# Kernel optimization log

Hardware: AMD Instinct MI355X
Metric: run time of the kernel (lower is better)

The kernel has to match this reference:

```python
import jax, jax.numpy as jnp
import numpy as np

INF, OUTF, BIT, GROUPSIZE = 4096, 11008, 4, 128
GROUPS = INF // GROUPSIZE  # 32
PACK = 32 // BIT           # 8 values per int32


def setup_inputs() -> dict:
    key = jax.random.key(0)
    k1, k2, k3, k4, k5 = jax.random.split(key, 5)
    x = jax.random.normal(k1, (2, 2048, INF), dtype=jnp.float32)
    # packed 4-bit weights: (INF*BIT/32, OUTF) int32
    qweight = jax.random.randint(k2, (INF * BIT // 32, OUTF), 0, 2147483647, dtype=jnp.int32)
    scales = jax.random.uniform(k3, (OUTF, GROUPS, 1), dtype=jnp.float32) * 0.01 + 0.001
    zeros = jax.random.uniform(k4, (OUTF, GROUPS, 1), dtype=jnp.float32) * 0.1
    bias = jax.random.normal(k5, (OUTF,), dtype=jnp.float32)
    return {"x": x, "qweight": qweight, "scales": scales, "zeros": zeros, "bias": bias}


def _dequant(qweight, scales, zeros):
    # unpack 8 nibbles per int32 row -> intweight (INF, OUTF)
    shifts = (BIT * jnp.arange(PACK, dtype=jnp.int32))[None, :, None]  # (1,8,1)
    nibbles = (qweight[:, None, :] >> shifts) & 0xF                    # (INF/8, 8, OUTF)
    wq = nibbles.reshape(INF, OUTF).astype(jnp.float32)
    # per-group dequant: W[k,n] = q*scale[n, k//gs] - zero[n, k//gs]
    s = scales[:, :, 0].T[:, None, :]  # (GROUPS, 1, OUTF)
    z = zeros[:, :, 0].T[:, None, :]
    w = wq.reshape(GROUPS, GROUPSIZE, OUTF) * s - z
    return w.reshape(INF, OUTF)


def reference(x, qweight, scales, zeros, bias):
    w = _dequant(qweight, scales, zeros)  # (INF, OUTF)
    # y = x @ W + bias  (matches y init to bias then vecquant4matmul accumulate)
    return jnp.einsum('bsk,kn->bsn', x, w) + bias
```

## Files before the change

### kernel.cpp

```cpp
#include <hip/hip_runtime.h>
#include <hip/hip_bf16.h>
#include <cstdint>
#include <cstddef>

#define K_DIM   4096
#define N_DIM   11008
#define M_DIM   4096
#define GROUPS  32
#define QROWS   512

typedef __bf16 bf16x8 __attribute__((ext_vector_type(8)));
typedef float  f32x4  __attribute__((ext_vector_type(4)));

__device__ __forceinline__ void async16(const void* g, void* lds) {
    __builtin_amdgcn_global_load_lds(
        (const __attribute__((address_space(1))) uint32_t*)g,
        (__attribute__((address_space(3))) uint32_t*)lds,
        16, 0, 0);
}

#define DQ_NN   64
#define DQ_KK   32
#define DQ_ROW  264
__global__ __launch_bounds__(256) void dequant_kernel(
        const uint32_t* __restrict__ qw,
        const float* __restrict__ scales,
        const float* __restrict__ zeros,
        __bf16* __restrict__ Wt) {
    __shared__ __align__(16) __bf16 T[DQ_NN * DQ_ROW];

    const int n0  = blockIdx.x * DQ_NN;
    const int kk0 = blockIdx.y * DQ_KK;
    const int tid = threadIdx.x;

#pragma unroll
    for (int it = 0; it < 8; ++it) {
        const int flat = it * 256 + tid;
        const int kk_l = flat >> 6;
        const int n_l  = flat & 63;
        const int kk   = kk0 + kk_l;
        const int n    = n0 + n_l;
        const uint32_t q = qw[(size_t)kk * N_DIM + n];
        const int g = kk >> 4;
        const float s = scales[(size_t)n * GROUPS + g];
        const float z = zeros[(size_t)n * GROUPS + g];
        bf16x8 w;
#pragma unroll
        for (int j = 0; j < 8; ++j) {
            float v = (float)((q >> (4 * j)) & 0xF) * s - z;
            w[j] = (__bf16)v;
        }
        *(bf16x8*)(&T[n_l * DQ_ROW + kk_l * 8]) = w;
    }
    __syncthreads();

#pragma unroll
    for (int it = 0; it < 8; ++it) {
        const int flat = it * 256 + tid;
        const int n_l    = flat >> 5;
        const int kchunk = flat & 31;
        bf16x8 v = *(const bf16x8*)(&T[n_l * DQ_ROW + kchunk * 8]);
        *(bf16x8*)(Wt + (size_t)(n0 + n_l) * K_DIM + (size_t)kk0 * 8 + kchunk * 8) = v;
    }
}

__global__ __launch_bounds__(256) void xconv_kernel(
        const float* __restrict__ x, __bf16* __restrict__ xb) {
    const size_t i = ((size_t)blockIdx.x * 256 + threadIdx.x) * 8;
    const float4* p = (const float4*)(x + i);
    float4 a = p[0];
    float4 b = p[1];
    bf16x8 o;
    o[0] = (__bf16)a.x; o[1] = (__bf16)a.y; o[2] = (__bf16)a.z; o[3] = (__bf16)a.w;
    o[4] = (__bf16)b.x; o[5] = (__bf16)b.y; o[6] = (__bf16)b.z; o[7] = (__bf16)b.w;
    *(bf16x8*)(xb + i) = o;
}

#define GN 86
#define GM 32
#define SN 16
__global__ __launch_bounds__(256, 4) void gemm_kernel(
        const __bf16* __restrict__ A,
        const __bf16* __restrict__ Bt,
        const float* __restrict__ bias,
        float* __restrict__ C) {
    __shared__ __align__(16) __bf16 As[128 * 32];
    __shared__ __align__(16) __bf16 Bs[128 * 32];

    const int tid  = threadIdx.x;
    const int wave = tid >> 6;
    const int lane = tid & 63;
    const int wm   = wave >> 1;
    const int wn   = wave & 1;
    const int quad = lane >> 4;
    const int l16  = lane & 15;

    const int bid = blockIdx.x;
    const int g   = bid >> 9;
    const int rem = bid & 511;
    int n_t, m_t;
    const int snw = (GN - g * SN) < SN ? (GN - g * SN) : SN;
    if (snw == SN) { n_t = g * SN + (rem & (SN - 1)); m_t = rem >> 4; }
    else           { n_t = g * SN + rem % snw;        m_t = rem / snw; }

    const int m0 = m_t * 128;
    const int n0 = n_t * 128;

    f32x4 acc[4][4] = {};

    const int c0 = wave * 128 + lane;
    const int c1 = c0 + 64;
    const __bf16* gA0 = A  + (size_t)(m0 + (c0 >> 2)) * K_DIM + (c0 & 3) * 8;
    const __bf16* gA1 = A  + (size_t)(m0 + (c1 >> 2)) * K_DIM + (c1 & 3) * 8;
    const __bf16* gB0 = Bt + (size_t)(n0 + (c0 >> 2)) * K_DIM + (c0 & 3) * 8;
    const __bf16* gB1 = Bt + (size_t)(n0 + (c1 >> 2)) * K_DIM + (c1 & 3) * 8;
    char* ldsA0 = (char*)As + (wave * 2 + 0) * 1024;
    char* ldsA1 = (char*)As + (wave * 2 + 1) * 1024;
    char* ldsB0 = (char*)Bs + (wave * 2 + 0) * 1024;
    char* ldsB1 = (char*)Bs + (wave * 2 + 1) * 1024;

    const __bf16* la = As + ((size_t)(wm * 64 + l16)) * 32 + quad * 8;
    const __bf16* lb = Bs + ((size_t)(wn * 64 + l16)) * 32 + quad * 8;

    for (int kt = 0; kt < K_DIM / 32; ++kt) {
        async16(gA0, ldsA0);
        async16(gA1, ldsA1);
        async16(gB0, ldsB0);
        async16(gB1, ldsB1);
        gA0 += 32; gA1 += 32; gB0 += 32; gB1 += 32;
        __syncthreads();

        bf16x8 af[4], bf[4];
#pragma unroll
        for (int i = 0; i < 4; ++i) af[i] = *(const bf16x8*)(la + i * 16 * 32);
#pragma unroll
        for (int i = 0; i < 4; ++i) bf[i] = *(const bf16x8*)(lb + i * 16 * 32);

#pragma unroll
        for (int i = 0; i < 4; ++i)
#pragma unroll
            for (int j = 0; j < 4; ++j)
                acc[i][j] = __builtin_amdgcn_mfma_f32_16x16x32_bf16(
                    af[i], bf[j], acc[i][j], 0, 0, 0);

        __syncthreads();
    }

#pragma unroll
    for (int j = 0; j < 4; ++j) {
        const int n = n0 + wn * 64 + j * 16 + l16;
        const float bv = bias[n];
#pragma unroll
        for (int i = 0; i < 4; ++i) {
            const int mb = m0 + wm * 64 + i * 16 + quad * 4;
#pragma unroll
            for (int r = 0; r < 4; ++r) {
                C[(size_t)(mb + r) * N_DIM + n] = acc[i][j][r] + bv;
            }
        }
    }
}

extern "C" void kernel_launch(void* const* d_in, const int* in_sizes, int n_in,
                              void* d_out, int out_size, void* d_ws, size_t ws_size,
                              hipStream_t stream) {
    const float*    x      = (const float*)d_in[0];
    const uint32_t* qw     = (const uint32_t*)d_in[1];
    const float*    scales = (const float*)d_in[2];
    const float*    zeros  = (const float*)d_in[3];
    const float*    bias   = (const float*)d_in[4];
    float*          out    = (float*)d_out;

    __bf16* Wt = (__bf16*)d_ws;
    __bf16* xb = (__bf16*)((char*)d_ws + (size_t)N_DIM * K_DIM * sizeof(__bf16));

    dim3 dq_grid(N_DIM / DQ_NN, QROWS / DQ_KK);
    dequant_kernel<<<dq_grid, 256, 0, stream>>>(qw, scales, zeros, Wt);
    xconv_kernel<<<(M_DIM * K_DIM) / (256 * 8), 256, 0, stream>>>(x, xb);

    gemm_kernel<<<GN * GM, 256, 0, stream>>>(xb, Wt, bias, out);
}
```

Baseline: 703.0 us.

## Rewrite GEMM with 256x256 tiles, double-buffered swizzled LDS and interleaved async staging

Replaces the 128x128x32 single-buffered GEMM with a 256x256x64 tile kernel using 8 waves. Global-to-LDS async loads for the next K-tile are spread across the MFMA phases, with explicit vmcnt waits and raw barriers, so memory traffic overlaps compute. LDS columns are XOR-swizzled to avoid bank conflicts, blocks are remapped across XCDs, and setprio raises MFMA priority. The larger tiles raise arithmetic intensity but use 128KB of LDS and many accumulator registers, which limits occupancy to a few blocks per CU.

```diff
diff --git a/kernel.cpp b/kernel.cpp
--- a/kernel.cpp
+++ b/kernel.cpp
@@ -18,6 +18,9 @@
         (__attribute__((address_space(3))) uint32_t*)lds,
         16, 0, 0);
 }
+
+#define FENCE() asm volatile("" ::: "memory")
+#define BAR()   do { FENCE(); __builtin_amdgcn_s_barrier(); FENCE(); } while (0)
 
 #define DQ_NN   64
 #define DQ_KK   32
@@ -76,87 +79,160 @@
     *(bf16x8*)(xb + i) = o;
 }
 
-#define GN 86
-#define GM 32
-#define SN 16
-__global__ __launch_bounds__(256, 4) void gemm_kernel(
+#define BM 256
+#define BN 256
+#define BK 64
+#define NT 43
+#define MT 16
+#define NWG (NT*MT)
+
+#define PH_BODY(MF, J0, J1)                                                   \
+    do {                                                                      \
+        bf16x8 aLk0 = *(const bf16x8*)(ar0 + (MF)*1024);                      \
+        bf16x8 aLk1 = *(const bf16x8*)(ar1 + (MF)*1024);                      \
+        bf16x8 aHk0 = *(const bf16x8*)(ar0 + ((MF)+1)*1024);                  \
+        bf16x8 aHk1 = *(const bf16x8*)(ar1 + ((MF)+1)*1024);                  \
+        if constexpr (DO_STAGE) {                                             \
+            async16(gsrc[(J0)], lds + ldst[(J0)] + soff);                     \
+            async16(gsrc[(J1)], lds + ldst[(J1)] + soff);                     \
+        }                                                                     \
+        BAR();                                                                \
+        __builtin_amdgcn_s_setprio(1);                                        \
+        acc[(MF)  ][0] = __builtin_amdgcn_mfma_f32_16x16x32_bf16(aLk0, b0k0, acc[(MF)  ][0], 0,0,0); \
+        acc[(MF)  ][1] = __builtin_amdgcn_mfma_f32_16x16x32_bf16(aLk0, b1k0, acc[(MF)  ][1], 0,0,0); \
+        acc[(MF)  ][2] = __builtin_amdgcn_mfma_f32_16x16x32_bf16(aLk0, b2k0, acc[(MF)  ][2], 0,0,0); \
+        acc[(MF)  ][3] = __builtin_amdgcn_mfma_f32_16x16x32_bf16(aLk0, b3k0, acc[(MF)  ][3], 0,0,0); \
+        acc[(MF)+1][0] = __builtin_amdgcn_mfma_f32_16x16x32_bf16(aHk0, b0k0, acc[(MF)+1][0], 0,0,0); \
+        acc[(MF)+1][1] = __builtin_amdgcn_mfma_f32_16x16x32_bf16(aHk0, b1k0, acc[(MF)+1][1], 0,0,0); \
+        acc[(MF)+1][2] = __builtin_amdgcn_mfma_f32_16x16x32_bf16(aHk0, b2k0, acc[(MF)+1][2], 0,0,0); \
+        acc[(MF)+1][3] = __builtin_amdgcn_mfma_f32_16x16x32_bf16(aHk0, b3k0, acc[(MF)+1][3], 0,0,0); \
+        acc[(MF)  ][0] = __builtin_amdgcn_mfma_f32_16x16x32_bf16(aLk1, b0k1, acc[(MF)  ][0], 0,0,0); \
+        acc[(MF)  ][1] = __builtin_amdgcn_mfma_f32_16x16x32_bf16(aLk1, b1k1, acc[(MF)  ][1], 0,0,0); \
+        acc[(MF)  ][2] = __builtin_amdgcn_mfma_f32_16x16x32_bf16(aLk1, b2k1, acc[(MF)  ][2], 0,0,0); \
+        acc[(MF)  ][3] = __builtin_amdgcn_mfma_f32_16x16x32_bf16(aLk1, b3k1, acc[(MF)  ][3], 0,0,0); \
+        acc[(MF)+1][0] = __builtin_amdgcn_mfma_f32_16x16x32_bf16(aHk1, b0k1, acc[(MF)+1][0], 0,0,0); \
+        acc[(MF)+1][1] = __builtin_amdgcn_mfma_f32_16x16x32_bf16(aHk1, b1k1, acc[(MF)+1][1], 0,0,0); \
+        acc[(MF)+1][2] = __builtin_amdgcn_mfma_f32_16x16x32_bf16(aHk1, b2k1, acc[(MF)+1][2], 0,0,0); \
+        acc[(MF)+1][3] = __builtin_amdgcn_mfma_f32_16x16x32_bf16(aHk1, b3k1, acc[(MF)+1][3], 0,0,0); \
+        __builtin_amdgcn_s_setprio(0);                                        \
+    } while (0)
+
+template<bool DO_STAGE>
+__device__ __forceinline__ void kgroup(
+        const __bf16* __restrict__ ar0, const __bf16* __restrict__ ar1,
+        const __bf16* __restrict__ br0, const __bf16* __restrict__ br1,
+        const __bf16* (&gsrc)[8], __bf16* lds, const int (&ldst)[8],
+        const int soff, f32x4 (&acc)[8][4])
+{
+    asm volatile("s_waitcnt vmcnt(2)" ::: "memory");
+    BAR();
+    bf16x8 b0k0 = *(const bf16x8*)(br0 + 0*1024);
+    bf16x8 b1k0 = *(const bf16x8*)(br0 + 1*1024);
+    bf16x8 b2k0 = *(const bf16x8*)(br0 + 2*1024);
+    bf16x8 b3k0 = *(const bf16x8*)(br0 + 3*1024);
+    bf16x8 b0k1 = *(const bf16x8*)(br1 + 0*1024);
+    bf16x8 b1k1 = *(const bf16x8*)(br1 + 1*1024);
+    bf16x8 b2k1 = *(const bf16x8*)(br1 + 2*1024);
+    bf16x8 b3k1 = *(const bf16x8*)(br1 + 3*1024);
+    PH_BODY(0, 0, 1);
+    BAR();
+    PH_BODY(2, 2, 3);
+    if constexpr (DO_STAGE) { asm volatile("s_waitcnt vmcnt(4)" ::: "memory"); }
+    else                    { asm volatile("s_waitcnt vmcnt(0)" ::: "memory"); }
+    BAR();
+    PH_BODY(4, 4, 5);
+    BAR();
+    PH_BODY(6, 6, 7);
+    if constexpr (DO_STAGE) {
+#pragma unroll
+        for (int j = 0; j < 8; ++j) gsrc[j] += BK;
+    }
+}
+
+__global__ __launch_bounds__(512, 2) void gemm_kernel(
         const __bf16* __restrict__ A,
         const __bf16* __restrict__ Bt,
         const float* __restrict__ bias,
         float* __restrict__ C) {
-    __shared__ __align__(16) __bf16 As[128 * 32];
-    __shared__ __align__(16) __bf16 Bs[128 * 32];
+    __shared__ __align__(16) __bf16 lds[65536];
 
     const int tid  = threadIdx.x;
     const int wave = tid >> 6;
     const int lane = tid & 63;
-    const int wm   = wave >> 1;
-    const int wn   = wave & 1;
+    const int wm   = wave >> 2;
+    const int wn   = wave & 3;
     const int quad = lane >> 4;
     const int l16  = lane & 15;
 
     const int bid = blockIdx.x;
-    const int g   = bid >> 9;
-    const int rem = bid & 511;
-    int n_t, m_t;
-    const int snw = (GN - g * SN) < SN ? (GN - g * SN) : SN;
-    if (snw == SN) { n_t = g * SN + (rem & (SN - 1)); m_t = rem >> 4; }
-    else           { n_t = g * SN + rem % snw;        m_t = rem / snw; }
-
-    const int m0 = m_t * 128;
-    const int n0 = n_t * 128;
-
-    f32x4 acc[4][4] = {};
-
-    const int c0 = wave * 128 + lane;
-    const int c1 = c0 + 64;
-    const __bf16* gA0 = A  + (size_t)(m0 + (c0 >> 2)) * K_DIM + (c0 & 3) * 8;
-    const __bf16* gA1 = A  + (size_t)(m0 + (c1 >> 2)) * K_DIM + (c1 & 3) * 8;
-    const __bf16* gB0 = Bt + (size_t)(n0 + (c0 >> 2)) * K_DIM + (c0 & 3) * 8;
-    const __bf16* gB1 = Bt + (size_t)(n0 + (c1 >> 2)) * K_DIM + (c1 & 3) * 8;
-    char* ldsA0 = (char*)As + (wave * 2 + 0) * 1024;
-    char* ldsA1 = (char*)As + (wave * 2 + 1) * 1024;
-    char* ldsB0 = (char*)Bs + (wave * 2 + 0) * 1024;
-    char* ldsB1 = (char*)Bs + (wave * 2 + 1) * 1024;
-
-    const __bf16* la = As + ((size_t)(wm * 64 + l16)) * 32 + quad * 8;
-    const __bf16* lb = Bs + ((size_t)(wn * 64 + l16)) * 32 + quad * 8;
-
-    for (int kt = 0; kt < K_DIM / 32; ++kt) {
-        async16(gA0, ldsA0);
-        async16(gA1, ldsA1);
-        async16(gB0, ldsB0);
-        async16(gB1, ldsB1);
-        gA0 += 32; gA1 += 32; gB0 += 32; gB1 += 32;
-        __syncthreads();
-
-        bf16x8 af[4], bf[4];
-#pragma unroll
-        for (int i = 0; i < 4; ++i) af[i] = *(const bf16x8*)(la + i * 16 * 32);
-#pragma unroll
-        for (int i = 0; i < 4; ++i) bf[i] = *(const bf16x8*)(lb + i * 16 * 32);
-
-#pragma unroll
-        for (int i = 0; i < 4; ++i)
-#pragma unroll
-            for (int j = 0; j < 4; ++j)
-                acc[i][j] = __builtin_amdgcn_mfma_f32_16x16x32_bf16(
-                    af[i], bf[j], acc[i][j], 0, 0, 0);
-
-        __syncthreads();
-    }
-
-#pragma unroll
-    for (int j = 0; j < 4; ++j) {
-        const int n = n0 + wn * 64 + j * 16 + l16;
+    const int swz = (bid & 7) * (NWG / 8) + (bid >> 3);
+    const int n_t = swz >> 4;
+    const int m_t = swz & 15;
+    const int m0 = m_t << 8;
+    const int n0 = n_t << 8;
+
+    f32x4 acc[8][4] = {};
+
+    const int srow = tid >> 3;
+    const int scol = ((tid & 7) ^ (srow & 7)) << 3;
+
+    const __bf16* gsrc[8];
+    gsrc[0] = A  + (size_t)(m0 +   0 + srow) * K_DIM + scol;
+    gsrc[1] = A  + (size_t)(m0 + 128 + srow) * K_DIM + scol;
+    gsrc[2] = Bt + (size_t)(n0 +   0 + srow) * K_DIM + scol;
+    gsrc[3] = Bt + (size_t)(n0 +  64 + srow) * K_DIM + scol;
+    gsrc[4] = Bt + (size_t)(n0 + 128 + srow) * K_DIM + scol;
+    gsrc[5] = Bt + (size_t)(n0 + 192 + srow) * K_DIM + scol;
+    gsrc[6] = A  + (size_t)(m0 +  64 + srow) * K_DIM + scol;
+    gsrc[7] = A  + (size_t)(m0 + 192 + srow) * K_DIM + scol;
+
+    const int wq = wave << 9;
+    const int ldst[8] = {
+        0*4096 + wq,          2*4096 + wq,
+        32768 + 0*4096 + wq,  32768 + 1*4096 + wq,
+        32768 + 2*4096 + wq,  32768 + 3*4096 + wq,
+        1*4096 + wq,          3*4096 + wq
+    };
+
+#pragma unroll
+    for (int j = 0; j < 8; ++j) async16(gsrc[j], lds + ldst[j]);
+#pragma unroll
+    for (int j = 0; j < 8; ++j) gsrc[j] += BK;
+
+    const int h3  = l16 & 7;
+    const int cc0 = (quad ^ h3) << 3;
+    const int cc1 = ((quad ^ h3) ^ 4) << 3;
+    const int arow = (wm << 7) + l16;
+    const int brow = (wn << 6) + l16;
+
+    const __bf16* a00 = lds + arow * 64 + cc0;
+    const __bf16* a01 = lds + arow * 64 + cc1;
+    const __bf16* b00 = lds + 32768 + brow * 64 + cc0;
+    const __bf16* b01 = lds + 32768 + brow * 64 + cc1;
+
+#pragma unroll 1
+    for (int gg = 0; gg < 31; ++gg) {
+        kgroup<true>(a00,         a01,         b00,         b01,
+                     gsrc, lds, ldst, 16384, acc);
+        kgroup<true>(a00 + 16384, a01 + 16384, b00 + 16384, b01 + 16384,
+                     gsrc, lds, ldst, 0,     acc);
+    }
+    kgroup<true >(a00,         a01,         b00,         b01,
+                  gsrc, lds, ldst, 16384, acc);
+    kgroup<false>(a00 + 16384, a01 + 16384, b00 + 16384, b01 + 16384,
+                  gsrc, lds, ldst, 0,     acc);
+
+#pragma unroll
+    for (int nf = 0; nf < 4; ++nf) {
+        const int n = n0 + (wn << 6) + (nf << 4) + l16;
         const float bv = bias[n];
 #pragma unroll
-        for (int i = 0; i < 4; ++i) {
-            const int mb = m0 + wm * 64 + i * 16 + quad * 4;
-#pragma unroll
-            for (int r = 0; r < 4; ++r) {
-                C[(size_t)(mb + r) * N_DIM + n] = acc[i][j][r] + bv;
-            }
+        for (int mf = 0; mf < 8; ++mf) {
+            const int mrow = m0 + (wm << 7) + (mf << 4) + (quad << 2);
+            float* cp = C + (size_t)mrow * N_DIM + n;
+#pragma unroll
+            for (int r = 0; r < 4; ++r)
+                cp[(size_t)r * N_DIM] = acc[mf][nf][r] + bv;
         }
     }
 }
@@ -178,5 +254,5 @@
     dequant_kernel<<<dq_grid, 256, 0, stream>>>(qw, scales, zeros, Wt);
     xconv_kernel<<<(M_DIM * K_DIM) / (256 * 8), 256, 0, stream>>>(x, xb);
 
-    gemm_kernel<<<GN * GM, 256, 0, stream>>>(xb, Wt, bias, out);
-}
+    gemm_kernel<<<NWG, 512, 0, stream>>>(xb, Wt, bias, out);
+}
```

Result: faster. 605.9 us (-13.8%).
